# Performance work log

Measured on AMD Instinct MI355X. Metric: run time of the kernel, lower is better.

Reference implementation:

```python
import jax, jax.numpy as jnp
import numpy as np

BOX = 256      # box_size
OS = 1         # oversampling
NC = 10        # n_classes
B = 16         # batch
N = 262144     # points per example


def setup_inputs() -> dict:
    key = jax.random.key(0)
    k1, k2 = jax.random.split(key)
    # coordinates in [-0.5, 0.5) so (points+0.5)*S lies inside the grid
    points = jax.random.uniform(k1, (B, 2, N), dtype=jnp.float32, minval=-0.5, maxval=0.5)
    values = jax.random.normal(k2, (B, NC, N), dtype=jnp.float32)
    return {"points": points, "values": values}


def reference(points, values):
    S = BOX * OS
    b, nc = points.shape[0], values.shape[1]
    # [B,2,N] -> [B,N,2], scaled into pixel coords
    p = jnp.swapaxes((points + 0.5) * S, 1, 2)
    xyf = jnp.floor(p)
    r = p - xyf                       # fractional part, [B,N,2]
    xy = xyf.astype(jnp.int32)
    x, y = xy[..., 0], xy[..., 1]     # [B,N]
    rx, ry = r[..., 0], r[..., 1]

    im = jnp.zeros((b, nc, S * S), dtype=values.dtype)

    def scat(acc, idx, contrib):
        # acc [NC, S*S], idx [N], contrib [NC, N]
        return acc.at[:, idx].add(contrib)

    scat_b = jax.vmap(scat)  # over batch

    # 4-corner bilinear (CIC) deposition
    for dx in (0, 1):
        x_ = x + dx
        wx = (1 - dx) + (2 * dx - 1) * rx
        for dy in (0, 1):
            y_ = y + dy
            wy = (1 - dy) + (2 * dy - 1) * ry
            valid = (x_ >= 0) & (x_ < S) & (y_ >= 0) & (y_ < S)
            idx = jnp.where(valid, y_ * S + x_, 0)           # [B,N]
            w = jnp.where(valid, wx * wy, 0.0)               # [B,N]
            im = scat_b(im, idx, w[:, None, :] * values)     # [B,NC,S*S]

    return im.reshape(b, nc, S, S)
```

## Files before the change

### kernel.cpp

```cpp
#include <hip/hip_runtime.h>

#define S_     256
#define NC_    10
#define CHUNK  1024
#define NBIN   256
#define CAP    1536
#define RSTR   7

typedef unsigned int u32;

__device__ __forceinline__ u32 f2bf(float f) {
    u32 u = __float_as_uint(f);
    return (u + 0x7fffu + ((u >> 16) & 1u)) >> 16;
}
__device__ __forceinline__ float bf2f(u32 h) { return __uint_as_float(h << 16); }


__global__ void __launch_bounds__(256)
k_hist(const float* __restrict__ points, u32* __restrict__ hist, int N) {
    __shared__ u32 h[NBIN];
    h[threadIdx.x] = 0;
    __syncthreads();
    const int cpb = N / CHUNK;
    const int b  = blockIdx.x / cpb;
    const int n0 = (blockIdx.x % cpb) * CHUNK;
    const float* pb = points + (size_t)b * 2 * N;
    for (int i = threadIdx.x; i < CHUNK; i += 256) {
        int n = n0 + i;
        float px = (pb[n] + 0.5f) * (float)S_;
        float py = (pb[(size_t)N + n] + 0.5f) * (float)S_;
        int xi = (int)floorf(px), yi = (int)floorf(py);
        int bin = ((yi >> 4) << 4) + (xi >> 4);
        atomicAdd(&h[bin], 1u);
    }
    __syncthreads();
    hist[(size_t)blockIdx.x * NBIN + threadIdx.x] = h[threadIdx.x];
}

__global__ void __launch_bounds__(256)
k_scan(const u32* __restrict__ hist, u32* __restrict__ blockStart,
       u32* __restrict__ binBase, u32* __restrict__ binCnt, int cpb, int N) {
    __shared__ u32 s[256];
    const int b = blockIdx.x, t = threadIdx.x;
    u32 tot = 0;
#pragma unroll 8
    for (int i = 0; i < cpb; ++i) tot += hist[(size_t)(b * cpb + i) * NBIN + t];
    s[t] = tot;
    __syncthreads();
    for (int off = 1; off < 256; off <<= 1) {
        u32 y = (t >= off) ? s[t - off] : 0;
        __syncthreads();
        s[t] += y;
        __syncthreads();
    }
    u32 base = (u32)b * (u32)N + s[t] - tot;
    binBase[b * NBIN + t] = base;
    binCnt[b * NBIN + t]  = tot;
    u32 run = base;
#pragma unroll 4
    for (int i = 0; i < cpb; ++i) {
        size_t idx = (size_t)(b * cpb + i) * NBIN + t;
        u32 hv = hist[idx];
        blockStart[idx] = run;
        run += hv;
    }
}

__global__ void __launch_bounds__(256)
k_scatter(const float* __restrict__ points, const float* __restrict__ values,
          const u32* __restrict__ blockStart, uint2* __restrict__ recs, int N) {
    __shared__ u32 cnt[NBIN];
    __shared__ u32 sc[NBIN];
    __shared__ u32 gOff[NBIN];
    __shared__ unsigned char binId[CHUNK];
    __shared__ u32 lw[6][CHUNK];

    const int tid = threadIdx.x;
    const int cpb = N / CHUNK;
    const int b  = blockIdx.x / cpb;
    const int n0 = (blockIdx.x % cpb) * CHUNK;
    const float* pb = points + (size_t)b * 2 * N;
    const float* vb = values + (size_t)b * NC_ * N;

    cnt[tid] = 0;
    __syncthreads();

    const int PPT = CHUNK / 256;
    u32 w0[PPT];
    u32 binArr[PPT];
#pragma unroll
    for (int k = 0; k < PPT; ++k) {
        int n = n0 + tid + k * 256;
        float px = (pb[n] + 0.5f) * (float)S_;
        float py = (pb[(size_t)N + n] + 0.5f) * (float)S_;
        int xi = (int)floorf(px), yi = (int)floorf(py);
        u32 qx = __float2uint_rn((px - (float)(xi & ~15)) * 2048.0f);
        u32 qy = __float2uint_rn((py - (float)(yi & ~15)) * 2048.0f);
        qx = min(qx, 32767u); qy = min(qy, 32767u);
        w0[k] = qx | (qy << 16);
        binArr[k] = (u32)(((yi >> 4) << 4) + (xi >> 4));
        atomicAdd(&cnt[binArr[k]], 1u);
    }
    __syncthreads();

    u32 c = cnt[tid];
    sc[tid] = c;
    __syncthreads();
    for (int off = 1; off < 256; off <<= 1) {
        u32 y = (tid >= off) ? sc[tid - off] : 0;
        __syncthreads();
        sc[tid] += y;
        __syncthreads();
    }
    u32 excl = sc[tid] - c;
    gOff[tid] = blockStart[(size_t)blockIdx.x * NBIN + tid] - excl;
    __syncthreads();
    cnt[tid] = excl;
    __syncthreads();

#pragma unroll
    for (int k = 0; k < PPT; ++k) {
        int n = n0 + tid + k * 256;
        float v[NC_];
#pragma unroll
        for (int cc = 0; cc < NC_; ++cc) v[cc] = vb[(size_t)cc * N + n];
        u32 bin = binArr[k];
        u32 slot = atomicAdd(&cnt[bin], 1u);
        binId[slot] = (unsigned char)bin;
        lw[0][slot] = w0[k];
        lw[1][slot] = f2bf(v[0]) | (f2bf(v[1]) << 16);
        lw[2][slot] = f2bf(v[2]) | (f2bf(v[3]) << 16);
        lw[3][slot] = f2bf(v[4]) | (f2bf(v[5]) << 16);
        lw[4][slot] = f2bf(v[6]) | (f2bf(v[7]) << 16);
        lw[5][slot] = f2bf(v[8]) | (f2bf(v[9]) << 16);
    }
    __syncthreads();

    for (int p = tid; p < CHUNK * 3; p += 256) {
        u32 r = (u32)p / 3u;
        u32 cidx = (u32)p - r * 3u;
        u32 dst = gOff[binId[r]] + r;
        recs[(size_t)dst * 3u + cidx] = make_uint2(lw[2 * cidx][r],
                                                   lw[2 * cidx + 1][r]);
    }
}

__global__ void __launch_bounds__(256)
k_fused(const uint2* __restrict__ recs, const u32* __restrict__ binBase,
        const u32* __restrict__ binCnt, float* __restrict__ out,
        float* __restrict__ borderBuf) {
    __shared__ u32 cnt[NBIN];
    __shared__ u32 excl[NBIN];
    __shared__ u32 sc[NBIN];
    __shared__ u32 lrec[CAP * RSTR];

    const int tid = threadIdx.x;
    const int g = blockIdx.x;
    const int batch = g >> 8, t = g & 255;
    const int ox = (t & 15) * 16, oy = (t >> 4) * 16;
    const u32 base = binBase[g];
    const u32 n = min(binCnt[g], (u32)CAP);

    cnt[tid] = 0;
    __syncthreads();

    u32 r[6][6];
    int cell[6];
#pragma unroll
    for (int k = 0; k < 6; ++k) {
        int i = k * 256 + tid;
        cell[k] = -1;
        if (i < (int)n) {
            size_t sa = (size_t)(base + i) * 3;
            uint2 a = recs[sa], b2 = recs[sa + 1], c2 = recs[sa + 2];
            r[k][0] = a.x;  r[k][1] = a.y;
            r[k][2] = b2.x; r[k][3] = b2.y;
            r[k][4] = c2.x; r[k][5] = c2.y;
            u32 qx = a.x & 0xffffu, qy = a.x >> 16;
            cell[k] = (int)(((qy >> 11) << 4) | (qx >> 11));
            atomicAdd(&cnt[cell[k]], 1u);
        }
    }
    __syncthreads();

    u32 c = cnt[tid];
    sc[tid] = c;
    __syncthreads();
    for (int off = 1; off < 256; off <<= 1) {
        u32 y = (tid >= off) ? sc[tid - off] : 0;
        __syncthreads();
        sc[tid] += y;
        __syncthreads();
    }
    excl[tid] = sc[tid] - c;
    __syncthreads();
    cnt[tid] = excl[tid];
    __syncthreads();

#pragma unroll
    for (int k = 0; k < 6; ++k) {
        if (cell[k] >= 0) {
            u32 o = atomicAdd(&cnt[cell[k]], 1u) * RSTR;
#pragma unroll
            for (int w = 0; w < 6; ++w) lrec[o + w] = r[k][w];
        }
    }
    __syncthreads();

    for (int p = tid; p < 289; p += 256) {
        int lx = p % 17, ly = p / 17;
        float acc[NC_];
#pragma unroll
        for (int q = 0; q < NC_; ++q) acc[q] = 0.0f;
#pragma unroll
        for (int dy = 0; dy < 2; ++dy) {
            int cy = ly - 1 + dy;
            if ((unsigned)cy >= 16u) continue;
#pragma unroll
            for (int dx = 0; dx < 2; ++dx) {
                int cx = lx - 1 + dx;
                if ((unsigned)cx >= 16u) continue;
                int cc = (cy << 4) | cx;
                u32 j1 = cnt[cc];
                for (u32 j = excl[cc]; j < j1; ++j) {
                    u32 o = j * RSTR;
                    u32 w0 = lrec[o];
                    float rx = (float)(w0 & 2047u)         * (1.0f / 2048.0f);
                    float ry = (float)((w0 >> 16) & 2047u) * (1.0f / 2048.0f);
                    float w = (dx ? (1.0f - rx) : rx) * (dy ? (1.0f - ry) : ry);
                    u32 w1 = lrec[o + 1], w2 = lrec[o + 2], w3 = lrec[o + 3],
                        w4 = lrec[o + 4], w5 = lrec[o + 5];
                    acc[0] += w * bf2f(w1 & 0xffffu); acc[1] += w * bf2f(w1 >> 16);
                    acc[2] += w * bf2f(w2 & 0xffffu); acc[3] += w * bf2f(w2 >> 16);
                    acc[4] += w * bf2f(w3 & 0xffffu); acc[5] += w * bf2f(w3 >> 16);
                    acc[6] += w * bf2f(w4 & 0xffffu); acc[7] += w * bf2f(w4 >> 16);
                    acc[8] += w * bf2f(w5 & 0xffffu); acc[9] += w * bf2f(w5 >> 16);
                }
            }
        }
        bool interior = (lx >= 1) & (lx <= 15) & (ly >= 1) & (ly <= 15);
        if (interior) {
            int gx = ox + lx, gy = oy + ly;
            float* ob = out + (size_t)batch * NC_ * S_ * S_ + gy * S_ + gx;
#pragma unroll
            for (int q = 0; q < NC_; ++q) ob[(size_t)q * S_ * S_] = acc[q];
        } else {
            float* bb = borderBuf + ((size_t)g * 289 + p) * NC_;
#pragma unroll
            for (int q = 0; q < NC_; ++q) bb[q] = acc[q];
        }
    }
}

__global__ void __launch_bounds__(256)
k_border(const float* __restrict__ borderBuf, float* __restrict__ out, int total) {
    int idx = blockIdx.x * 256 + threadIdx.x;
    if (idx >= total) return;
    int b = idx / 7936;
    int j = idx - b * 7936;
    int gx, gy;
    if (j < 4096) {
        gx = (j >> 8) << 4;
        gy = j & 255;
    } else {
        int j2 = j - 4096;
        int row = j2 / 240, col = j2 - row * 240;
        gy = row << 4;
        gx = col + 1 + col / 15;
    }

    int txs[2], lxs[2], nx = 0;
    bool bx = (gx & 15) == 0, by = (gy & 15) == 0;
    if (bx) {
        if (gx > 0) { txs[nx] = (gx >> 4) - 1; lxs[nx] = 16; ++nx; }
        txs[nx] = gx >> 4; lxs[nx] = 0; ++nx;
    } else { txs[0] = gx >> 4; lxs[0] = gx & 15; nx = 1; }
    int tys[2], lys[2], ny = 0;
    if (by) {
        if (gy > 0) { tys[ny] = (gy >> 4) - 1; lys[ny] = 16; ++ny; }
        tys[ny] = gy >> 4; lys[ny] = 0; ++ny;
    } else { tys[0] = gy >> 4; lys[0] = gy & 15; ny = 1; }

    float acc[NC_];
#pragma unroll
    for (int q = 0; q < NC_; ++q) acc[q] = 0.0f;
    for (int jj = 0; jj < ny; ++jj)
        for (int ii = 0; ii < nx; ++ii) {
            int g = (b << 8) + (tys[jj] << 4) + txs[ii];
            int p = lys[jj] * 17 + lxs[ii];
            const float* bb = borderBuf + ((size_t)g * 289 + p) * NC_;
#pragma unroll
            for (int q = 0; q < NC_; ++q) acc[q] += bb[q];
        }
    float* ob = out + (size_t)b * NC_ * S_ * S_ + gy * S_ + gx;
#pragma unroll
    for (int q = 0; q < NC_; ++q) ob[(size_t)q * S_ * S_] = acc[q];
}

__global__ void __launch_bounds__(256)
k_cleanup(const uint2* __restrict__ recs, const u32* __restrict__ binBase,
          const u32* __restrict__ binCnt, float* __restrict__ out, int nTiles) {
    int g = blockIdx.x * 256 + threadIdx.x;
    if (g >= nTiles) return;
    u32 n = binCnt[g];
    if (n <= (u32)CAP) return;
    int batch = g >> 8, t = g & 255;
    int ox = (t & 15) * 16, oy = (t >> 4) * 16;
    u32 base = binBase[g];
    float* ob = out + (size_t)batch * NC_ * S_ * S_;
    for (u32 i = CAP; i < n; ++i) {
        size_t sa = (size_t)(base + i) * 3;
        uint2 a = recs[sa], b2 = recs[sa + 1], c2 = recs[sa + 2];
        u32 qx = a.x & 0xffffu, qy = a.x >> 16;
        int xi = ox + (int)(qx >> 11), yi = oy + (int)(qy >> 11);
        float rx = (float)(qx & 2047u) * (1.0f / 2048.0f);
        float ry = (float)(qy & 2047u) * (1.0f / 2048.0f);
        float v[NC_];
        v[0] = bf2f(a.y & 0xffffu);  v[1] = bf2f(a.y >> 16);
        v[2] = bf2f(b2.x & 0xffffu); v[3] = bf2f(b2.x >> 16);
        v[4] = bf2f(b2.y & 0xffffu); v[5] = bf2f(b2.y >> 16);
        v[6] = bf2f(c2.x & 0xffffu); v[7] = bf2f(c2.x >> 16);
        v[8] = bf2f(c2.y & 0xffffu); v[9] = bf2f(c2.y >> 16);
        for (int dx = 0; dx < 2; ++dx) {
            int x_ = xi + dx; if (x_ >= S_) continue;
            float wx = dx ? rx : (1.0f - rx);
            for (int dy = 0; dy < 2; ++dy) {
                int y_ = yi + dy; if (y_ >= S_) continue;
                float w = wx * (dy ? ry : (1.0f - ry));
                for (int c = 0; c < NC_; ++c)
                    atomicAdd(ob + (size_t)c * S_ * S_ + y_ * S_ + x_, w * v[c]);
            }
        }
    }
}

__global__ void __launch_bounds__(256)
scatter_cic_kernel(const float* __restrict__ points,
                   const float* __restrict__ values,
                   float* __restrict__ out, int N) {
    const int n = blockIdx.x * blockDim.x + threadIdx.x;
    const int b = blockIdx.y;
    if (n >= N) return;
    const float* pb = points + (size_t)b * 2 * N;
    const float px = (pb[n] + 0.5f) * (float)S_;
    const float py = (pb[(size_t)N + n] + 0.5f) * (float)S_;
    const float xf = floorf(px), yf = floorf(py);
    const float rx = px - xf, ry = py - yf;
    const int xi = (int)xf, yi = (int)yf;
    const float* vb = values + (size_t)b * NC_ * N + n;
    float v[NC_];
#pragma unroll
    for (int c = 0; c < NC_; ++c) v[c] = vb[(size_t)c * N];
    float* ob = out + (size_t)b * NC_ * S_ * S_;
#pragma unroll
    for (int dx = 0; dx < 2; ++dx) {
        const int x_ = xi + dx;
        if (x_ < 0 || x_ >= S_) continue;
        const float wx = dx ? rx : (1.0f - rx);
#pragma unroll
        for (int dy = 0; dy < 2; ++dy) {
            const int y_ = yi + dy;
            if (y_ < 0 || y_ >= S_) continue;
            const float w = wx * (dy ? ry : (1.0f - ry));
            const int idx = y_ * S_ + x_;
#pragma unroll
            for (int c = 0; c < NC_; ++c)
                atomicAdd(ob + (size_t)c * S_ * S_ + idx, w * v[c]);
        }
    }
}

extern "C" void kernel_launch(void* const* d_in, const int* in_sizes, int n_in,
                              void* d_out, int out_size, void* d_ws, size_t ws_size,
                              hipStream_t stream) {
    const float* points = (const float*)d_in[0];
    const float* values = (const float*)d_in[1];
    float* out = (float*)d_out;

    const int B = out_size / (NC_ * S_ * S_);
    const int N = in_sizes[0] / (2 * B);

    const size_t P = (size_t)B * N;
    const int cpb = N / CHUNK;
    const int chunksTotal = B * cpb;
    const int nTiles = B * NBIN;

    const size_t recBytes    = P * 24;
    const size_t histElems   = (size_t)chunksTotal * NBIN;
    const size_t borderElems = (size_t)nTiles * 289 * NC_;
    const size_t wsNeeded    = recBytes + 2 * histElems * 4 +
                               2 * (size_t)nTiles * 4 + borderElems * 4 + 256;

    const bool fast = (N % CHUNK == 0) && (N >= CHUNK) && (B > 0) &&
                      (P < (1u << 31) / 2) && (ws_size >= wsNeeded);

    if (fast) {
        char* w = (char*)d_ws;
        uint2* recsA     = (uint2*)w;
        u32* hist        = (u32*)(w + recBytes);
        u32* blockStart  = hist + histElems;
        u32* binBase     = blockStart + histElems;
        u32* binCnt      = binBase + nTiles;
        float* borderBuf = (float*)(binCnt + nTiles);

        k_hist<<<chunksTotal, 256, 0, stream>>>(points, hist, N);
        k_scan<<<B, 256, 0, stream>>>(hist, blockStart, binBase, binCnt, cpb, N);
        k_scatter<<<chunksTotal, 256, 0, stream>>>(points, values, blockStart, recsA, N);
        k_fused<<<nTiles, 256, 0, stream>>>(recsA, binBase, binCnt, out, borderBuf);
        const int borderTotal = B * 7936;
        k_border<<<(borderTotal + 255) / 256, 256, 0, stream>>>(borderBuf, out, borderTotal);
        k_cleanup<<<(nTiles + 255) / 256, 256, 0, stream>>>(recsA, binBase, binCnt, out, nTiles);
    } else {
        hipMemsetAsync(d_out, 0, (size_t)out_size * sizeof(float), stream);
        dim3 block(256, 1, 1);
        dim3 grid((N + 255) / 256, B, 1);
        scatter_cic_kernel<<<grid, block, 0, stream>>>(points, values, out, N);
    }
}
```

Measured before the change: 415.8 us.

## Replace histogram+scan binning with fixed-capacity per-tile buckets via atomic cursors

Measured after the change: 389.2 us. 6.4% less time.

```diff
diff --git a/kernel.cpp b/kernel.cpp
--- a/kernel.cpp
+++ b/kernel.cpp
@@ -4,6 +4,7 @@
 #define NC_    10
 #define CHUNK  1024
 #define NBIN   256
+#define CAPR   1536
 #define CAP    1536
 #define RSTR   7
 
@@ -17,61 +18,12 @@
 
 
 __global__ void __launch_bounds__(256)
-k_hist(const float* __restrict__ points, u32* __restrict__ hist, int N) {
-    __shared__ u32 h[NBIN];
-    h[threadIdx.x] = 0;
-    __syncthreads();
-    const int cpb = N / CHUNK;
-    const int b  = blockIdx.x / cpb;
-    const int n0 = (blockIdx.x % cpb) * CHUNK;
-    const float* pb = points + (size_t)b * 2 * N;
-    for (int i = threadIdx.x; i < CHUNK; i += 256) {
-        int n = n0 + i;
-        float px = (pb[n] + 0.5f) * (float)S_;
-        float py = (pb[(size_t)N + n] + 0.5f) * (float)S_;
-        int xi = (int)floorf(px), yi = (int)floorf(py);
-        int bin = ((yi >> 4) << 4) + (xi >> 4);
-        atomicAdd(&h[bin], 1u);
-    }
-    __syncthreads();
-    hist[(size_t)blockIdx.x * NBIN + threadIdx.x] = h[threadIdx.x];
-}
-
-__global__ void __launch_bounds__(256)
-k_scan(const u32* __restrict__ hist, u32* __restrict__ blockStart,
-       u32* __restrict__ binBase, u32* __restrict__ binCnt, int cpb, int N) {
-    __shared__ u32 s[256];
-    const int b = blockIdx.x, t = threadIdx.x;
-    u32 tot = 0;
-#pragma unroll 8
-    for (int i = 0; i < cpb; ++i) tot += hist[(size_t)(b * cpb + i) * NBIN + t];
-    s[t] = tot;
-    __syncthreads();
-    for (int off = 1; off < 256; off <<= 1) {
-        u32 y = (t >= off) ? s[t - off] : 0;
-        __syncthreads();
-        s[t] += y;
-        __syncthreads();
-    }
-    u32 base = (u32)b * (u32)N + s[t] - tot;
-    binBase[b * NBIN + t] = base;
-    binCnt[b * NBIN + t]  = tot;
-    u32 run = base;
-#pragma unroll 4
-    for (int i = 0; i < cpb; ++i) {
-        size_t idx = (size_t)(b * cpb + i) * NBIN + t;
-        u32 hv = hist[idx];
-        blockStart[idx] = run;
-        run += hv;
-    }
-}
-
-__global__ void __launch_bounds__(256)
 k_scatter(const float* __restrict__ points, const float* __restrict__ values,
-          const u32* __restrict__ blockStart, uint2* __restrict__ recs, int N) {
+          u32* __restrict__ cursor, u32* __restrict__ ovfCnt,
+          u32* __restrict__ ovfBuf, uint2* __restrict__ recs, int N) {
     __shared__ u32 cnt[NBIN];
-    __shared__ u32 sc[NBIN];
     __shared__ u32 gOff[NBIN];
+    __shared__ u32 wsum[4];
     __shared__ unsigned char binId[CHUNK];
     __shared__ u32 lw[6][CHUNK];
 
@@ -81,85 +33,111 @@
     const int n0 = (blockIdx.x % cpb) * CHUNK;
     const float* pb = points + (size_t)b * 2 * N;
     const float* vb = values + (size_t)b * NC_ * N;
+    const int nb = n0 + tid * 4;
 
     cnt[tid] = 0;
-    __syncthreads();
-
-    const int PPT = CHUNK / 256;
-    u32 w0[PPT];
-    u32 binArr[PPT];
-#pragma unroll
-    for (int k = 0; k < PPT; ++k) {
-        int n = n0 + tid + k * 256;
-        float px = (pb[n] + 0.5f) * (float)S_;
-        float py = (pb[(size_t)N + n] + 0.5f) * (float)S_;
+
+    const float4 pxv = *(const float4*)(pb + nb);
+    const float4 pyv = *(const float4*)(pb + (size_t)N + nb);
+    float4 vv[NC_];
+#pragma unroll
+    for (int c = 0; c < NC_; ++c)
+        vv[c] = *(const float4*)(vb + (size_t)c * N + nb);
+
+    __syncthreads();
+
+    float px4[4] = {pxv.x, pxv.y, pxv.z, pxv.w};
+    float py4[4] = {pyv.x, pyv.y, pyv.z, pyv.w};
+    u32 w0[4], binA[4];
+#pragma unroll
+    for (int k = 0; k < 4; ++k) {
+        float px = (px4[k] + 0.5f) * (float)S_;
+        float py = (py4[k] + 0.5f) * (float)S_;
         int xi = (int)floorf(px), yi = (int)floorf(py);
         u32 qx = __float2uint_rn((px - (float)(xi & ~15)) * 2048.0f);
         u32 qy = __float2uint_rn((py - (float)(yi & ~15)) * 2048.0f);
         qx = min(qx, 32767u); qy = min(qy, 32767u);
         w0[k] = qx | (qy << 16);
-        binArr[k] = (u32)(((yi >> 4) << 4) + (xi >> 4));
-        atomicAdd(&cnt[binArr[k]], 1u);
-    }
-    __syncthreads();
-
-    u32 c = cnt[tid];
-    sc[tid] = c;
-    __syncthreads();
-    for (int off = 1; off < 256; off <<= 1) {
-        u32 y = (tid >= off) ? sc[tid - off] : 0;
-        __syncthreads();
-        sc[tid] += y;
-        __syncthreads();
-    }
-    u32 excl = sc[tid] - c;
-    gOff[tid] = blockStart[(size_t)blockIdx.x * NBIN + tid] - excl;
-    __syncthreads();
+        binA[k] = (u32)(((yi >> 4) << 4) + (xi >> 4));
+        atomicAdd(&cnt[binA[k]], 1u);
+    }
+    __syncthreads();
+
+    u32 myCnt = cnt[tid];
+    u32 x = myCnt;
+#pragma unroll
+    for (int off = 1; off < 64; off <<= 1) {
+        u32 y = __shfl_up(x, off, 64);
+        if ((tid & 63) >= off) x += y;
+    }
+    if ((tid & 63) == 63) wsum[tid >> 6] = x;
+    __syncthreads();
+    u32 add = 0;
+#pragma unroll
+    for (int w = 0; w < 4; ++w) add += (w < (tid >> 6)) ? wsum[w] : 0;
+    u32 excl = x - myCnt + add;
+
+    const u32 gt = (u32)b * NBIN + (u32)tid;
+    u32 gbase = 0;
+    if (myCnt) gbase = gt * (u32)CAPR + atomicAdd(&cursor[gt], myCnt);
+    gOff[tid] = gbase - excl;
     cnt[tid] = excl;
     __syncthreads();
 
 #pragma unroll
-    for (int k = 0; k < PPT; ++k) {
-        int n = n0 + tid + k * 256;
-        float v[NC_];
-#pragma unroll
-        for (int cc = 0; cc < NC_; ++cc) v[cc] = vb[(size_t)cc * N + n];
-        u32 bin = binArr[k];
+    for (int k = 0; k < 4; ++k) {
+        u32 bin = binA[k];
         u32 slot = atomicAdd(&cnt[bin], 1u);
         binId[slot] = (unsigned char)bin;
+#define VG(c) ((&vv[c].x)[k])
         lw[0][slot] = w0[k];
-        lw[1][slot] = f2bf(v[0]) | (f2bf(v[1]) << 16);
-        lw[2][slot] = f2bf(v[2]) | (f2bf(v[3]) << 16);
-        lw[3][slot] = f2bf(v[4]) | (f2bf(v[5]) << 16);
-        lw[4][slot] = f2bf(v[6]) | (f2bf(v[7]) << 16);
-        lw[5][slot] = f2bf(v[8]) | (f2bf(v[9]) << 16);
-    }
-    __syncthreads();
-
-    for (int p = tid; p < CHUNK * 3; p += 256) {
-        u32 r = (u32)p / 3u;
-        u32 cidx = (u32)p - r * 3u;
-        u32 dst = gOff[binId[r]] + r;
-        recs[(size_t)dst * 3u + cidx] = make_uint2(lw[2 * cidx][r],
-                                                   lw[2 * cidx + 1][r]);
+        lw[1][slot] = f2bf(VG(0)) | (f2bf(VG(1)) << 16);
+        lw[2][slot] = f2bf(VG(2)) | (f2bf(VG(3)) << 16);
+        lw[3][slot] = f2bf(VG(4)) | (f2bf(VG(5)) << 16);
+        lw[4][slot] = f2bf(VG(6)) | (f2bf(VG(7)) << 16);
+        lw[5][slot] = f2bf(VG(8)) | (f2bf(VG(9)) << 16);
+#undef VG
+    }
+    __syncthreads();
+
+    const u32 tb0 = (u32)b * NBIN;
+#pragma unroll
+    for (int k = 0; k < 4; ++k) {
+        u32 r = (u32)tid + (u32)k * 256;
+        u32 bin = binId[r];
+        u32 dst = gOff[bin] + r;
+        u32 a0 = lw[0][r], a1 = lw[1][r], a2 = lw[2][r],
+            a3 = lw[3][r], a4 = lw[4][r], a5 = lw[5][r];
+        u32 rel = dst - (tb0 + bin) * (u32)CAPR;
+        if (rel < (u32)CAPR) {
+            size_t s3 = (size_t)dst * 3;
+            recs[s3]     = make_uint2(a0, a1);
+            recs[s3 + 1] = make_uint2(a2, a3);
+            recs[s3 + 2] = make_uint2(a4, a5);
+        } else {
+            u32 oi = atomicAdd(ovfCnt, 1u);
+            u32* ob = ovfBuf + (size_t)oi * 7;
+            ob[0] = tb0 + bin;
+            ob[1] = a0; ob[2] = a1; ob[3] = a2;
+            ob[4] = a3; ob[5] = a4; ob[6] = a5;
+        }
     }
 }
 
 __global__ void __launch_bounds__(256)
-k_fused(const uint2* __restrict__ recs, const u32* __restrict__ binBase,
-        const u32* __restrict__ binCnt, float* __restrict__ out,
-        float* __restrict__ borderBuf) {
+k_fused(const uint2* __restrict__ recs, const u32* __restrict__ cursor,
+        float* __restrict__ out, float* __restrict__ borderBuf) {
     __shared__ u32 cnt[NBIN];
     __shared__ u32 excl[NBIN];
-    __shared__ u32 sc[NBIN];
+    __shared__ u32 wsum[4];
     __shared__ u32 lrec[CAP * RSTR];
 
     const int tid = threadIdx.x;
     const int g = blockIdx.x;
     const int batch = g >> 8, t = g & 255;
     const int ox = (t & 15) * 16, oy = (t >> 4) * 16;
-    const u32 base = binBase[g];
-    const u32 n = min(binCnt[g], (u32)CAP);
+    const u32 base = (u32)g * (u32)CAPR;
+    const u32 n = min(cursor[g], (u32)CAP);
 
     cnt[tid] = 0;
     __syncthreads();
@@ -184,17 +162,20 @@
     __syncthreads();
 
     u32 c = cnt[tid];
-    sc[tid] = c;
-    __syncthreads();
-    for (int off = 1; off < 256; off <<= 1) {
-        u32 y = (tid >= off) ? sc[tid - off] : 0;
-        __syncthreads();
-        sc[tid] += y;
-        __syncthreads();
-    }
-    excl[tid] = sc[tid] - c;
-    __syncthreads();
-    cnt[tid] = excl[tid];
+    u32 x = c;
+#pragma unroll
+    for (int off = 1; off < 64; off <<= 1) {
+        u32 y = __shfl_up(x, off, 64);
+        if ((tid & 63) >= off) x += y;
+    }
+    if ((tid & 63) == 63) wsum[tid >> 6] = x;
+    __syncthreads();
+    u32 add = 0;
+#pragma unroll
+    for (int w = 0; w < 4; ++w) add += (w < (tid >> 6)) ? wsum[w] : 0;
+    u32 ex = x - c + add;
+    excl[tid] = ex;
+    cnt[tid] = ex;
     __syncthreads();
 
 #pragma unroll
@@ -252,10 +233,45 @@
     }
 }
 
+#define CLEAN_T 4096
 __global__ void __launch_bounds__(256)
-k_border(const float* __restrict__ borderBuf, float* __restrict__ out, int total) {
+k_border(const float* __restrict__ borderBuf, float* __restrict__ out,
+         const u32* __restrict__ ovfCnt, const u32* __restrict__ ovfBuf,
+         int total) {
     int idx = blockIdx.x * 256 + threadIdx.x;
-    if (idx >= total) return;
+    if (idx >= total) {
+        u32 oc = *ovfCnt;
+        for (u32 j = (u32)(idx - total); j < oc; j += CLEAN_T) {
+            const u32* ob = ovfBuf + (size_t)j * 7;
+            u32 g = ob[0];
+            int batch = (int)(g >> 8), t = (int)(g & 255u);
+            int ox = (t & 15) * 16, oy = (t >> 4) * 16;
+            u32 w0 = ob[1];
+            u32 qx = w0 & 0xffffu, qy = w0 >> 16;
+            int xi = ox + (int)(qx >> 11), yi = oy + (int)(qy >> 11);
+            float rx = (float)(qx & 2047u) * (1.0f / 2048.0f);
+            float ry = (float)(qy & 2047u) * (1.0f / 2048.0f);
+            float v[NC_];
+            v[0] = bf2f(ob[2] & 0xffffu); v[1] = bf2f(ob[2] >> 16);
+            v[2] = bf2f(ob[3] & 0xffffu); v[3] = bf2f(ob[3] >> 16);
+            v[4] = bf2f(ob[4] & 0xffffu); v[5] = bf2f(ob[4] >> 16);
+            v[6] = bf2f(ob[5] & 0xffffu); v[7] = bf2f(ob[5] >> 16);
+            v[8] = bf2f(ob[6] & 0xffffu); v[9] = bf2f(ob[6] >> 16);
+            float* obase = out + (size_t)batch * NC_ * S_ * S_;
+            for (int dx = 0; dx < 2; ++dx) {
+                int x_ = xi + dx; if (x_ >= S_) continue;
+                float wx = dx ? rx : (1.0f - rx);
+                for (int dy = 0; dy < 2; ++dy) {
+                    int y_ = yi + dy; if (y_ >= S_) continue;
+                    float w = wx * (dy ? ry : (1.0f - ry));
+                    for (int cc = 0; cc < NC_; ++cc)
+                        atomicAdd(obase + (size_t)cc * S_ * S_ + y_ * S_ + x_,
+                                  w * v[cc]);
+                }
+            }
+        }
+        return;
+    }
     int b = idx / 7936;
     int j = idx - b * 7936;
     int gx, gy;
@@ -295,43 +311,6 @@
     float* ob = out + (size_t)b * NC_ * S_ * S_ + gy * S_ + gx;
 #pragma unroll
     for (int q = 0; q < NC_; ++q) ob[(size_t)q * S_ * S_] = acc[q];
-}
-
-__global__ void __launch_bounds__(256)
-k_cleanup(const uint2* __restrict__ recs, const u32* __restrict__ binBase,
-          const u32* __restrict__ binCnt, float* __restrict__ out, int nTiles) {
-    int g = blockIdx.x * 256 + threadIdx.x;
-    if (g >= nTiles) return;
-    u32 n = binCnt[g];
-    if (n <= (u32)CAP) return;
-    int batch = g >> 8, t = g & 255;
-    int ox = (t & 15) * 16, oy = (t >> 4) * 16;
-    u32 base = binBase[g];
-    float* ob = out + (size_t)batch * NC_ * S_ * S_;
-    for (u32 i = CAP; i < n; ++i) {
-        size_t sa = (size_t)(base + i) * 3;
-        uint2 a = recs[sa], b2 = recs[sa + 1], c2 = recs[sa + 2];
-        u32 qx = a.x & 0xffffu, qy = a.x >> 16;
-        int xi = ox + (int)(qx >> 11), yi = oy + (int)(qy >> 11);
-        float rx = (float)(qx & 2047u) * (1.0f / 2048.0f);
-        float ry = (float)(qy & 2047u) * (1.0f / 2048.0f);
-        float v[NC_];
-        v[0] = bf2f(a.y & 0xffffu);  v[1] = bf2f(a.y >> 16);
-        v[2] = bf2f(b2.x & 0xffffu); v[3] = bf2f(b2.x >> 16);
-        v[4] = bf2f(b2.y & 0xffffu); v[5] = bf2f(b2.y >> 16);
-        v[6] = bf2f(c2.x & 0xffffu); v[7] = bf2f(c2.x >> 16);
-        v[8] = bf2f(c2.y & 0xffffu); v[9] = bf2f(c2.y >> 16);
-        for (int dx = 0; dx < 2; ++dx) {
-            int x_ = xi + dx; if (x_ >= S_) continue;
-            float wx = dx ? rx : (1.0f - rx);
-            for (int dy = 0; dy < 2; ++dy) {
-                int y_ = yi + dy; if (y_ >= S_) continue;
-                float w = wx * (dy ? ry : (1.0f - ry));
-                for (int c = 0; c < NC_; ++c)
-                    atomicAdd(ob + (size_t)c * S_ * S_ + y_ * S_ + x_, w * v[c]);
-            }
-        }
-    }
 }
 
 __global__ void __launch_bounds__(256)
@@ -385,11 +364,11 @@
     const int chunksTotal = B * cpb;
     const int nTiles = B * NBIN;
 
-    const size_t recBytes    = P * 24;
-    const size_t histElems   = (size_t)chunksTotal * NBIN;
+    const size_t recBytes    = (size_t)nTiles * CAPR * 24;
     const size_t borderElems = (size_t)nTiles * 289 * NC_;
-    const size_t wsNeeded    = recBytes + 2 * histElems * 4 +
-                               2 * (size_t)nTiles * 4 + borderElems * 4 + 256;
+    const size_t ovfBytes    = P * 7 * 4;
+    const size_t wsNeeded    = recBytes + (size_t)(nTiles + 1) * 4 +
+                               borderElems * 4 + ovfBytes + 256;
 
     const bool fast = (N % CHUNK == 0) && (N >= CHUNK) && (B > 0) &&
                       (P < (1u << 31) / 2) && (ws_size >= wsNeeded);
@@ -397,19 +376,18 @@
     if (fast) {
         char* w = (char*)d_ws;
         uint2* recsA     = (uint2*)w;
-        u32* hist        = (u32*)(w + recBytes);
-        u32* blockStart  = hist + histElems;
-        u32* binBase     = blockStart + histElems;
-        u32* binCnt      = binBase + nTiles;
-        float* borderBuf = (float*)(binCnt + nTiles);
-
-        k_hist<<<chunksTotal, 256, 0, stream>>>(points, hist, N);
-        k_scan<<<B, 256, 0, stream>>>(hist, blockStart, binBase, binCnt, cpb, N);
-        k_scatter<<<chunksTotal, 256, 0, stream>>>(points, values, blockStart, recsA, N);
-        k_fused<<<nTiles, 256, 0, stream>>>(recsA, binBase, binCnt, out, borderBuf);
+        u32* cursor      = (u32*)(w + recBytes);
+        u32* ovfCnt      = cursor + nTiles;
+        float* borderBuf = (float*)(ovfCnt + 1);
+        u32* ovfBuf      = (u32*)(borderBuf + borderElems);
+
+        hipMemsetAsync(cursor, 0, (size_t)(nTiles + 1) * 4, stream);
+        k_scatter<<<chunksTotal, 256, 0, stream>>>(points, values, cursor,
+                                                   ovfCnt, ovfBuf, recsA, N);
+        k_fused<<<nTiles, 256, 0, stream>>>(recsA, cursor, out, borderBuf);
         const int borderTotal = B * 7936;
-        k_border<<<(borderTotal + 255) / 256, 256, 0, stream>>>(borderBuf, out, borderTotal);
-        k_cleanup<<<(nTiles + 255) / 256, 256, 0, stream>>>(recsA, binBase, binCnt, out, nTiles);
+        k_border<<<borderTotal / 256 + CLEAN_T / 256, 256, 0, stream>>>(
+            borderBuf, out, ovfCnt, ovfBuf, borderTotal);
     } else {
         hipMemsetAsync(d_out, 0, (size_t)out_size * sizeof(float), stream);
         dim3 block(256, 1, 1);
```
